# Optimization experiments

Measured on AMD Instinct MI355X. Metric: run time of the kernel, lower is better.

The kernel has to match this reference:

```python
import jax, jax.numpy as jnp
import numpy as np

B, S, N, F, H, E = 1, 32, 2048, 64, 128, 32768


def setup_inputs() -> dict:
    key = jax.random.key(0)
    ks = jax.random.split(key, 13)
    p = lambda k, shp: (jax.random.normal(k, shp, dtype=jnp.float32) * 0.05)
    return {
        "x": jax.random.normal(ks[0], (B, S, N, F), dtype=jnp.float32),
        "edge_indexs": jax.random.randint(ks[1], (1, 2, S * E), 0, N, dtype=jnp.int64),
        "edgenum": E,
        "W1": p(ks[2], (F, H)), "b1": p(ks[3], (H,)),
        "W2": p(ks[4], (H, H)), "b2": p(ks[5], (H,)),
        "Wrel": p(ks[6], (H, H)), "brel": p(ks[7], (H,)),
        "Wroot": p(ks[8], (H, H)),
        "W3": p(ks[9], (H, H)), "b3": p(ks[10], (H,)),
        "W4": p(ks[11], (H, 1)), "b4": p(ks[12], (1,)),
    }


def reference(x, edge_indexs, edgenum, W1, b1, W2, b2, Wrel, brel, Wroot, W3, b3, W4, b4):
    batch, seq_len, num_stocks, _ = x.shape
    lrelu = jax.nn.leaky_relu  # default slope 0.01, matches nn.LeakyReLU()
    h = lrelu(x @ W1 + b1)
    h = lrelu(h @ W2 + b2)                       # [B,S,N,H]
    h = h.reshape(seq_len, num_stocks, -1)       # batch==1
    # split of [2, S*E] along edge dim into per-timestep graphs
    edges = edge_indexs[0].reshape(2, seq_len, edgenum)

    def step(h_t, src, tgt):
        # GraphConv(aggr='mean'): lin_rel(mean_j x_j) + lin_root(x_i)
        agg = jax.ops.segment_sum(h_t[src], tgt, num_segments=num_stocks)
        cnt = jax.ops.segment_sum(jnp.ones((edgenum,), h_t.dtype), tgt,
                                  num_segments=num_stocks)
        agg = agg / jnp.maximum(cnt, 1.0)[:, None]
        # all gnn layers share weights and each re-reads output[i], so one
        # application reproduces the original loop's final `out` exactly
        return lrelu(agg @ Wrel + brel + h_t @ Wroot)

    gnn_out = jax.vmap(step)(h, edges[0], edges[1])          # [S,N,H]
    out = gnn_out.reshape(batch, seq_len, num_stocks, -1)
    out = lrelu(out @ W3 + b3)
    out = out @ W4 + b4                                      # [B,S,N,1]
    return out[:, -1].reshape(batch, num_stocks, -1)
```

## Files before the change

kernel.cpp:

```cpp
#include <hip/hip_runtime.h>


#define N_NODES 2048
#define F_IN 64
#define H_DIM 128
#define S_LEN 32
#define E_EDGES 32768
#define T_LAST (S_LEN - 1)
#define CAP 96
#define NBLK 256
#define TPB 1024

__device__ __forceinline__ float lrelu(float v) { return v > 0.0f ? v : 0.01f * v; }

__global__ __launch_bounds__(TPB) void kA(
    const float* __restrict__ x, const int* __restrict__ ei,
    const float* __restrict__ W1, const float* __restrict__ b1,
    const float* __restrict__ W2, const float* __restrict__ b2,
    int* __restrict__ deg, int* __restrict__ bucket, float* __restrict__ h2)
{
    __shared__ float xs[8][F_IN];
    __shared__ float h1s[8][H_DIM];
    __shared__ float ws[16 * H_DIM];
    const int t = threadIdx.x;
    const int bid = blockIdx.x;
    const int node0 = bid * 8;

    if (t < 128) {
        const int e = bid * 128 + t;
        const int src = ei[(size_t)T_LAST * E_EDGES + e];
        const int tgt = ei[(size_t)(S_LEN + T_LAST) * E_EDGES + e];
        const int slot = atomicAdd(&deg[tgt], 1);
        if (slot < CAP) bucket[tgt * CAP + slot] = src;
    }

    if (t < 512)
        ((float*)xs)[t] = x[((size_t)T_LAST * N_NODES + node0) * F_IN + t];

    const int n = t >> 7;
    const int j = t & 127;

    float a0 = b1[j], a1 = 0.f;
    for (int kt = 0; kt < 4; ++kt) {
        __syncthreads();
        ((float2*)ws)[t] = ((const float2*)(W1 + kt * 16 * H_DIM))[t];
        __syncthreads();
        #pragma unroll
        for (int r = 0; r < 16; r += 2) {
            const int k = kt * 16 + r;
            a0 += xs[n][k]     * ws[r * H_DIM + j];
            a1 += xs[n][k + 1] * ws[(r + 1) * H_DIM + j];
        }
    }
    __syncthreads();
    h1s[n][j] = lrelu(a0 + a1);

    float c0 = b2[j], c1 = 0.f;
    for (int kt = 0; kt < 8; ++kt) {
        __syncthreads();
        ((float2*)ws)[t] = ((const float2*)(W2 + kt * 16 * H_DIM))[t];
        __syncthreads();
        #pragma unroll
        for (int r = 0; r < 16; r += 2) {
            const int k = kt * 16 + r;
            c0 += h1s[n][k]     * ws[r * H_DIM + j];
            c1 += h1s[n][k + 1] * ws[(r + 1) * H_DIM + j];
        }
    }
    h2[(size_t)(node0 + n) * H_DIM + j] = lrelu(c0 + c1);
}

__global__ __launch_bounds__(TPB) void kB(
    const float* __restrict__ h2,
    const int* __restrict__ deg, const int* __restrict__ bucket,
    const float* __restrict__ Wrel, const float* __restrict__ brel,
    const float* __restrict__ Wroot,
    const float* __restrict__ W3, const float* __restrict__ b3,
    const float* __restrict__ W4, const float* __restrict__ b4,
    float* __restrict__ out)
{
    __shared__ float h2s[8][H_DIM];
    __shared__ float aggs[8][H_DIM];
    __shared__ float gs[8][H_DIM];
    __shared__ float ws[2][16 * H_DIM];
    __shared__ int   bl[8][CAP];
    __shared__ float pred[16];
    const int t = threadIdx.x;
    const int node0 = blockIdx.x * 8;
    const int n = t >> 7;
    const int j = t & 127;

    h2s[n][j] = h2[(size_t)(node0 + n) * H_DIM + j];
    const int dg = min(deg[node0 + n], CAP);
    if (j < dg) bl[n][j] = bucket[(node0 + n) * CAP + j];
    __syncthreads();

    float a0 = 0.f, a1 = 0.f, a2 = 0.f, a3 = 0.f;
    int i = 0;
    for (; i + 3 < dg; i += 4) {
        const int s0 = bl[n][i], s1 = bl[n][i + 1], s2 = bl[n][i + 2], s3 = bl[n][i + 3];
        a0 += h2[(size_t)s0 * H_DIM + j];
        a1 += h2[(size_t)s1 * H_DIM + j];
        a2 += h2[(size_t)s2 * H_DIM + j];
        a3 += h2[(size_t)s3 * H_DIM + j];
    }
    for (; i < dg; ++i) a0 += h2[(size_t)bl[n][i] * H_DIM + j];
    aggs[n][j] = ((a0 + a1) + (a2 + a3)) / fmaxf((float)dg, 1.0f);

    float g0 = brel[j], g1 = 0.f;
    for (int kt = 0; kt < 8; ++kt) {
        __syncthreads();
        if (t < 512)
            ((float4*)ws[0])[t] = ((const float4*)(Wrel + kt * 16 * H_DIM))[t];
        else
            ((float4*)ws[1])[t - 512] = ((const float4*)(Wroot + kt * 16 * H_DIM))[t - 512];
        __syncthreads();
        #pragma unroll
        for (int r = 0; r < 16; r += 2) {
            const int k = kt * 16 + r;
            g0 += aggs[n][k]     * ws[0][r * H_DIM + j]
                + h2s[n][k]      * ws[1][r * H_DIM + j];
            g1 += aggs[n][k + 1] * ws[0][(r + 1) * H_DIM + j]
                + h2s[n][k + 1]  * ws[1][(r + 1) * H_DIM + j];
        }
    }
    __syncthreads();
    gs[n][j] = lrelu(g0 + g1);

    float h0 = b3[j], h1 = 0.f;
    for (int kt = 0; kt < 8; ++kt) {
        __syncthreads();
        ((float2*)ws[0])[t] = ((const float2*)(W3 + kt * 16 * H_DIM))[t];
        __syncthreads();
        #pragma unroll
        for (int r = 0; r < 16; r += 2) {
            const int k = kt * 16 + r;
            h0 += gs[n][k]     * ws[0][r * H_DIM + j];
            h1 += gs[n][k + 1] * ws[0][(r + 1) * H_DIM + j];
        }
    }
    float p = lrelu(h0 + h1) * W4[j];

    for (int off = 32; off >= 1; off >>= 1) p += __shfl_down(p, off);
    if ((t & 63) == 0) pred[t >> 6] = p;
    __syncthreads();
    if (t < 8)
        out[node0 + t] = pred[2 * t] + pred[2 * t + 1] + b4[0];
}

extern "C" void kernel_launch(void* const* d_in, const int* in_sizes, int n_in,
                              void* d_out, int out_size, void* d_ws, size_t ws_size,
                              hipStream_t stream)
{
    const float* x     = (const float*)d_in[0];
    const int*   ei    = (const int*)d_in[1];
    const float* W1    = (const float*)d_in[3];
    const float* b1    = (const float*)d_in[4];
    const float* W2    = (const float*)d_in[5];
    const float* b2    = (const float*)d_in[6];
    const float* Wrel  = (const float*)d_in[7];
    const float* brel  = (const float*)d_in[8];
    const float* Wroot = (const float*)d_in[9];
    const float* W3    = (const float*)d_in[10];
    const float* b3    = (const float*)d_in[11];
    const float* W4    = (const float*)d_in[12];
    const float* b4    = (const float*)d_in[13];
    float* out = (float*)d_out;

    int*   deg    = (int*)d_ws;
    int*   bucket = deg + N_NODES;
    float* h2     = (float*)(bucket + (size_t)N_NODES * CAP);

    hipMemsetAsync(deg, 0, N_NODES * sizeof(int), stream);
    kA<<<NBLK, TPB, 0, stream>>>(x, ei, W1, b1, W2, b2, deg, bucket, h2);
    kB<<<NBLK, TPB, 0, stream>>>(h2, deg, bucket, Wrel, brel, Wroot,
                                 W3, b3, W4, b4, out);
}
```

Measured before the change: 125.1 us.

## Halve nodes per block and double-buffer weight tiles in shared memory

Blocks now process 4 nodes with 512 threads, and twice as many blocks are launched to spread work over more CUs. Weight tiles for every matmul stage are double-buffered in shared memory: the next tile is loaded while the current one is consumed, which removes one barrier per tile. Kernel A uses 32-row tiles and prefetches W2 during the W1 stage. Kernel B prefetches W3 during the last GraphConv tile. More blocks each re-read the full weight matrices, which adds global/L2 weight traffic per node.

```diff
diff --git a/kernel.cpp b/kernel.cpp
--- a/kernel.cpp
+++ b/kernel.cpp
@@ -8,8 +8,9 @@
 #define E_EDGES 32768
 #define T_LAST (S_LEN - 1)
 #define CAP 96
-#define NBLK 256
-#define TPB 1024
+#define NBLK 512
+#define TPB 512
+#define NPB 4
 
 __device__ __forceinline__ float lrelu(float v) { return v > 0.0f ? v : 0.01f * v; }
 
@@ -19,52 +20,64 @@
     const float* __restrict__ W2, const float* __restrict__ b2,
     int* __restrict__ deg, int* __restrict__ bucket, float* __restrict__ h2)
 {
-    __shared__ float xs[8][F_IN];
-    __shared__ float h1s[8][H_DIM];
-    __shared__ float ws[16 * H_DIM];
+    __shared__ float xs[NPB][F_IN];
+    __shared__ float h1s[NPB][H_DIM];
+    __shared__ float ws[2][32 * H_DIM];
     const int t = threadIdx.x;
     const int bid = blockIdx.x;
-    const int node0 = bid * 8;
-
-    if (t < 128) {
-        const int e = bid * 128 + t;
+    const int node0 = bid * NPB;
+
+    if (t < 64) {
+        const int e = bid * 64 + t;
         const int src = ei[(size_t)T_LAST * E_EDGES + e];
         const int tgt = ei[(size_t)(S_LEN + T_LAST) * E_EDGES + e];
         const int slot = atomicAdd(&deg[tgt], 1);
         if (slot < CAP) bucket[tgt * CAP + slot] = src;
     }
 
-    if (t < 512)
+    if (t < 256)
         ((float*)xs)[t] = x[((size_t)T_LAST * N_NODES + node0) * F_IN + t];
 
     const int n = t >> 7;
     const int j = t & 127;
 
+    ((float4*)ws[0])[t]       = ((const float4*)(W1))[t];
+    ((float4*)ws[0])[t + 512] = ((const float4*)(W1))[t + 512];
+
     float a0 = b1[j], a1 = 0.f;
+    __syncthreads();
+    ((float4*)ws[1])[t]       = ((const float4*)(W1 + 32 * H_DIM))[t];
+    ((float4*)ws[1])[t + 512] = ((const float4*)(W1 + 32 * H_DIM))[t + 512];
+    #pragma unroll
+    for (int r = 0; r < 32; r += 2) {
+        a0 += xs[n][r]     * ws[0][r * H_DIM + j];
+        a1 += xs[n][r + 1] * ws[0][(r + 1) * H_DIM + j];
+    }
+    __syncthreads();
+    ((float4*)ws[0])[t]       = ((const float4*)(W2))[t];
+    ((float4*)ws[0])[t + 512] = ((const float4*)(W2))[t + 512];
+    #pragma unroll
+    for (int r = 0; r < 32; r += 2) {
+        a0 += xs[n][32 + r]     * ws[1][r * H_DIM + j];
+        a1 += xs[n][32 + r + 1] * ws[1][(r + 1) * H_DIM + j];
+    }
+    h1s[n][j] = lrelu(a0 + a1);
+
+    float c0 = b2[j], c1 = 0.f;
     for (int kt = 0; kt < 4; ++kt) {
         __syncthreads();
-        ((float2*)ws)[t] = ((const float2*)(W1 + kt * 16 * H_DIM))[t];
-        __syncthreads();
+        if (kt < 3) {
+            ((float4*)ws[(kt + 1) & 1])[t] =
+                ((const float4*)(W2 + (kt + 1) * 32 * H_DIM))[t];
+            ((float4*)ws[(kt + 1) & 1])[t + 512] =
+                ((const float4*)(W2 + (kt + 1) * 32 * H_DIM))[t + 512];
+        }
+        const float* wb = ws[kt & 1];
         #pragma unroll
-        for (int r = 0; r < 16; r += 2) {
-            const int k = kt * 16 + r;
-            a0 += xs[n][k]     * ws[r * H_DIM + j];
-            a1 += xs[n][k + 1] * ws[(r + 1) * H_DIM + j];
-        }
-    }
-    __syncthreads();
-    h1s[n][j] = lrelu(a0 + a1);
-
-    float c0 = b2[j], c1 = 0.f;
-    for (int kt = 0; kt < 8; ++kt) {
-        __syncthreads();
-        ((float2*)ws)[t] = ((const float2*)(W2 + kt * 16 * H_DIM))[t];
-        __syncthreads();
-        #pragma unroll
-        for (int r = 0; r < 16; r += 2) {
-            const int k = kt * 16 + r;
-            c0 += h1s[n][k]     * ws[r * H_DIM + j];
-            c1 += h1s[n][k + 1] * ws[(r + 1) * H_DIM + j];
+        for (int r = 0; r < 32; r += 2) {
+            const int k = kt * 32 + r;
+            c0 += h1s[n][k]     * wb[r * H_DIM + j];
+            c1 += h1s[n][k + 1] * wb[(r + 1) * H_DIM + j];
         }
     }
     h2[(size_t)(node0 + n) * H_DIM + j] = lrelu(c0 + c1);
@@ -79,20 +92,24 @@
     const float* __restrict__ W4, const float* __restrict__ b4,
     float* __restrict__ out)
 {
-    __shared__ float h2s[8][H_DIM];
-    __shared__ float aggs[8][H_DIM];
-    __shared__ float gs[8][H_DIM];
-    __shared__ float ws[2][16 * H_DIM];
-    __shared__ int   bl[8][CAP];
-    __shared__ float pred[16];
+    __shared__ float h2s[NPB][H_DIM];
+    __shared__ float aggs[NPB][H_DIM];
+    __shared__ float gs[NPB][H_DIM];
+    __shared__ float wsA[2][16 * H_DIM];
+    __shared__ float wsB[2][16 * H_DIM];
+    __shared__ int   bl[NPB][CAP];
+    __shared__ float pred[8];
     const int t = threadIdx.x;
-    const int node0 = blockIdx.x * 8;
+    const int node0 = blockIdx.x * NPB;
     const int n = t >> 7;
     const int j = t & 127;
 
     h2s[n][j] = h2[(size_t)(node0 + n) * H_DIM + j];
     const int dg = min(deg[node0 + n], CAP);
     if (j < dg) bl[n][j] = bucket[(node0 + n) * CAP + j];
+
+    ((float4*)wsA[0])[t] = ((const float4*)(Wrel))[t];
+    ((float4*)wsB[0])[t] = ((const float4*)(Wroot))[t];
     __syncthreads();
 
     float a0 = 0.f, a1 = 0.f, a2 = 0.f, a3 = 0.f;
@@ -106,45 +123,51 @@
     }
     for (; i < dg; ++i) a0 += h2[(size_t)bl[n][i] * H_DIM + j];
     aggs[n][j] = ((a0 + a1) + (a2 + a3)) / fmaxf((float)dg, 1.0f);
+    __syncthreads();
 
     float g0 = brel[j], g1 = 0.f;
     for (int kt = 0; kt < 8; ++kt) {
-        __syncthreads();
-        if (t < 512)
-            ((float4*)ws[0])[t] = ((const float4*)(Wrel + kt * 16 * H_DIM))[t];
-        else
-            ((float4*)ws[1])[t - 512] = ((const float4*)(Wroot + kt * 16 * H_DIM))[t - 512];
-        __syncthreads();
+        if (kt < 7) {
+            ((float4*)wsA[(kt + 1) & 1])[t] =
+                ((const float4*)(Wrel + (kt + 1) * 16 * H_DIM))[t];
+            ((float4*)wsB[(kt + 1) & 1])[t] =
+                ((const float4*)(Wroot + (kt + 1) * 16 * H_DIM))[t];
+        } else {
+            ((float4*)wsA[(kt + 1) & 1])[t] = ((const float4*)(W3))[t];
+        }
+        const float* wa = wsA[kt & 1];
+        const float* wb = wsB[kt & 1];
         #pragma unroll
         for (int r = 0; r < 16; r += 2) {
             const int k = kt * 16 + r;
-            g0 += aggs[n][k]     * ws[0][r * H_DIM + j]
-                + h2s[n][k]      * ws[1][r * H_DIM + j];
-            g1 += aggs[n][k + 1] * ws[0][(r + 1) * H_DIM + j]
-                + h2s[n][k + 1]  * ws[1][(r + 1) * H_DIM + j];
-        }
-    }
-    __syncthreads();
+            g0 += aggs[n][k]     * wa[r * H_DIM + j] + h2s[n][k]     * wb[r * H_DIM + j];
+            g1 += aggs[n][k + 1] * wa[(r + 1) * H_DIM + j] + h2s[n][k + 1] * wb[(r + 1) * H_DIM + j];
+        }
+        __syncthreads();
+    }
     gs[n][j] = lrelu(g0 + g1);
+    __syncthreads();
 
     float h0 = b3[j], h1 = 0.f;
     for (int kt = 0; kt < 8; ++kt) {
-        __syncthreads();
-        ((float2*)ws[0])[t] = ((const float2*)(W3 + kt * 16 * H_DIM))[t];
-        __syncthreads();
+        if (kt < 7)
+            ((float4*)wsA[(kt + 1) & 1])[t] =
+                ((const float4*)(W3 + (kt + 1) * 16 * H_DIM))[t];
+        const float* wa = wsA[kt & 1];
         #pragma unroll
         for (int r = 0; r < 16; r += 2) {
             const int k = kt * 16 + r;
-            h0 += gs[n][k]     * ws[0][r * H_DIM + j];
-            h1 += gs[n][k + 1] * ws[0][(r + 1) * H_DIM + j];
-        }
+            h0 += gs[n][k]     * wa[r * H_DIM + j];
+            h1 += gs[n][k + 1] * wa[(r + 1) * H_DIM + j];
+        }
+        __syncthreads();
     }
     float p = lrelu(h0 + h1) * W4[j];
 
     for (int off = 32; off >= 1; off >>= 1) p += __shfl_down(p, off);
     if ((t & 63) == 0) pred[t >> 6] = p;
     __syncthreads();
-    if (t < 8)
+    if (t < NPB)
         out[node0 + t] = pred[2 * t] + pred[2 * t + 1] + b4[0];
 }
 
```

New measurement: 118.7 us. -5.1%, faster.
